# Kernel optimization log

Hardware: AMD Instinct MI355X
Metric: run time of the kernel (lower is better)

The kernel has to match this reference:

```python
import jax, jax.numpy as jnp
import numpy as np

B, S, HID = 2, 4096, 1024
H, D = 16, 64

def rotate_half(x):
    x1, x2 = jnp.split(x, 2, axis=-1)
    return jnp.concatenate([-x2, x1], axis=-1)

def setup_inputs() -> dict:
    key = jax.random.key(0)
    ks = jax.random.split(key, 8)
    hidden_states = jax.random.normal(ks[0], (B, S, HID), dtype=jnp.float32)
    pos = jnp.arange(S, dtype=jnp.float32)[:, None]
    inv_freq = 1.0 / (10000.0 ** (jnp.arange(0, D, 2, dtype=jnp.float32) / D))
    freqs = pos * inv_freq[None, :]
    emb = jnp.concatenate([freqs, freqs], axis=-1)  # [S, D]
    cos = jnp.cos(emb)
    sin = jnp.sin(emb)
    W_rkv = jax.random.normal(ks[1], (3 * H * D, HID), dtype=jnp.float32) * 0.02
    W_o = jax.random.normal(ks[2], (HID, H * D), dtype=jnp.float32) * 0.02
    # match torch init: uniform(-8,-5), uniform(-1,1), uniform(0.2,0.8)
    time_decay = jax.random.uniform(ks[3], (H, D), minval=-8.0, maxval=-5.0, dtype=jnp.float32)
    time_first = jax.random.uniform(ks[4], (H, D), minval=-1.0, maxval=1.0, dtype=jnp.float32)
    time_mix = jax.random.uniform(ks[5], (1, 1, HID), minval=0.2, maxval=0.8, dtype=jnp.float32)
    return {"hidden_states": hidden_states, "cos": cos, "sin": sin,
            "W_rkv": W_rkv, "W_o": W_o, "time_decay": time_decay,
            "time_first": time_first, "time_mix": time_mix}

def reference(hidden_states, cos, sin, W_rkv, W_o, time_decay, time_first, time_mix):
    b, s, hid = hidden_states.shape
    # token-shift time mixing
    xx = jnp.concatenate([jnp.zeros_like(hidden_states[:, :1]), hidden_states[:, :-1]], axis=1)
    mixed = hidden_states * time_mix + xx * (1.0 - time_mix)
    rkv = jnp.einsum('bsh,oh->bso', mixed, W_rkv).reshape(b, s, 3, H, D)
    r = jax.nn.sigmoid(rkv[:, :, 0])  # [B,S,H,D]
    k = rkv[:, :, 1]
    v = rkv[:, :, 2]
    # rotary on r, k
    c = cos[None, :, None, :]
    sn = sin[None, :, None, :]
    r = r * c + rotate_half(r) * sn
    k = k * c + rotate_half(k) * sn
    # fast rwkv linear attention (parallel approximation)
    w = -jnp.exp(time_decay)
    kv = k * v  # [B,S,H,D]
    pos = jnp.arange(s, dtype=hidden_states.dtype)
    pos_diff = pos[:, None] - pos[None, :]  # [S,S]
    mask = pos_diff > 0  # i > j masked (per original code)
    avg_decay = jnp.mean(w)
    pd = jnp.where(mask, 0.0, pos_diff)
    dw = jnp.where(mask, 0.0, jnp.exp(avg_decay * -jnp.abs(pd)))
    dw = dw / (dw.sum(axis=1, keepdims=True) + 1e-8)
    weighted_kv = jnp.einsum('ij,bjhd->bihd', dw, kv)
    out = r * (time_first[None, None] * kv + weighted_kv)  # [B,S,H,D]
    out = out.reshape(b, s, H * D)
    return jnp.einsum('bso,ho->bsh', out, W_o)
```

## Files before the change

### kernel.cpp

```cpp
#include <hip/hip_runtime.h>
#include <math.h>

#define S_LEN 4096
#define HIDN  1024
#define NH    16
#define HD    64
#define BATCH 2
#define M_TOTAL (BATCH * S_LEN)
#define N_RKV   (3 * HIDN)
#define CS 128
#define NC (S_LEN / CS)

typedef __attribute__((ext_vector_type(8))) _Float16 f16x8;
typedef __attribute__((ext_vector_type(4))) float f32x4;
typedef __attribute__((ext_vector_type(4))) unsigned short u16x4;

__device__ __forceinline__ unsigned short f2h(float x) {
    _Float16 h = (_Float16)x;
    return *(unsigned short*)&h;
}
__device__ __forceinline__ float h2f(unsigned short b) {
    _Float16 h = *(_Float16*)&b;
    return (float)h;
}

__device__ __forceinline__ void load_lds16(const void* g, void* l) {
    __builtin_amdgcn_global_load_lds((const __attribute__((address_space(1))) void*)g,
                                     (__attribute__((address_space(3))) void*)l, 16, 0, 0);
}

__global__ __launch_bounds__(256)
void k_split_mix(const float* __restrict__ hs, const float* __restrict__ tm,
                 unsigned short* __restrict__ Ah) {
    int g = blockIdx.x * 256 + threadIdx.x;
    int kc = (g & 255) * 4;
    int m = g >> 8;
    float4 cur = *(const float4*)&hs[(size_t)m * HIDN + kc];
    float4 t4  = *(const float4*)&tm[kc];
    float4 prev = make_float4(0.f, 0.f, 0.f, 0.f);
    if (m & (S_LEN - 1)) prev = *(const float4*)&hs[(size_t)(m - 1) * HIDN + kc];
    u16x4 h;
    h.x = f2h(cur.x * t4.x + prev.x * (1.f - t4.x));
    h.y = f2h(cur.y * t4.y + prev.y * (1.f - t4.y));
    h.z = f2h(cur.z * t4.z + prev.z * (1.f - t4.z));
    h.w = f2h(cur.w * t4.w + prev.w * (1.f - t4.w));
    *(u16x4*)&Ah[(size_t)m * HIDN + kc] = h;
}

__global__ __launch_bounds__(256)
void k_prep_w(const float* __restrict__ Wr, unsigned short* __restrict__ Wrh,
              const float* __restrict__ Wo, unsigned short* __restrict__ Woh,
              const float* __restrict__ td, float* __restrict__ a_out) {
    int bid = blockIdx.x;
    if (bid < 4096) {
        const float* src = (bid < 3072) ? Wr : Wo;
        unsigned short* dst = (bid < 3072) ? Wrh : Woh;
        int g = ((bid < 3072) ? bid : (bid - 3072)) * 256 + threadIdx.x;
        size_t o = (size_t)g * 4;
        float4 v = *(const float4*)&src[o];
        u16x4 h;
        h.x = f2h(v.x); h.y = f2h(v.y); h.z = f2h(v.z); h.w = f2h(v.w);
        *(u16x4*)&dst[o] = h;
    } else if (threadIdx.x < 64) {
        int t = threadIdx.x;
        double acc = 0.0;
        for (int i = t; i < NH * HD; i += 64) acc += exp((double)td[i]);
        for (int off = 32; off > 0; off >>= 1) acc += __shfl_down(acc, off, 64);
        if (t == 0) a_out[0] = (float)(acc / (double)(NH * HD));
    }
}

__device__ __forceinline__ f32x4 mfma16(f16x8 a, f16x8 b, f32x4 c) {
    return __builtin_amdgcn_mfma_f32_16x16x32_f16(a, b, c, 0, 0, 0);
}

#define SBAR  do { __builtin_amdgcn_sched_barrier(0); __builtin_amdgcn_s_barrier(); \
                   __builtin_amdgcn_sched_barrier(0); } while (0)
#define LGKM0 do { asm volatile("s_waitcnt lgkmcnt(0)" ::: "memory"); \
                   __builtin_amdgcn_sched_barrier(0); } while (0)
#define VMC(n) asm volatile("s_waitcnt vmcnt(" #n ")" ::: "memory")

__global__ __launch_bounds__(512, 2)
void k_gemm1_8ph(const unsigned short* __restrict__ A,
                 const unsigned short* __restrict__ Bm,
                 unsigned short* __restrict__ C)
{
    __shared__ unsigned short smem[57344];
    const int tid  = threadIdx.x;
    const int lane = tid & 63;
    const int wv   = tid >> 6;
    const int wm = wv >> 2, wn = wv & 3;
    const int lm = lane & 15, rq = lane >> 4;
    const int swz = (lm & 7) << 4;

    const int cpx = gridDim.x >> 3;
    const int wg  = (blockIdx.x & 7) * cpx + (blockIdx.x >> 3);
    const int bx  = wg & 15;
    const int by  = wg >> 4;
    const int m0 = by * 256, n0 = bx * 192;

    const int srow = 8 * wv + (lane >> 3);
    const int scol = ((lane & 7) ^ (lane >> 3)) * 8;
    const unsigned short* sA = A  + (size_t)(m0 + srow) * 1024 + scol;
    const unsigned short* sB = Bm + (size_t)(n0 + srow) * 1024 + scol;
    unsigned short* dA = smem + wv * 512;
    unsigned short* dB = smem + 16384 + wv * 512;

#define STG_A(u, T, bf) load_lds16(sA + (u)*65536 + (T)*64, dA + (bf)*28672 + (u)*4096)
#define STG_B(u, T, bf) load_lds16(sB + (u)*65536 + (T)*64, dB + (bf)*28672 + (u)*4096)

    const int arow = (wm * 128 + lm) * 128 + rq * 16;
    int boff[3][2];
#pragma unroll
    for (int nt = 0; nt < 3; ++nt)
#pragma unroll
        for (int kk = 0; kk < 2; ++kk)
            boff[nt][kk] = (((wn * 48 + nt * 16 + lm) * 128 + rq * 16 + kk * 64) ^ swz);

    f16x8 aF[2][2], bF[3][2];
    f32x4 acc[8][3] = {};

#define READ_A(q, bf) { const char* Ab = (const char*)smem + (bf)*57344; \
    _Pragma("unroll") for (int m2 = 0; m2 < 2; ++m2) \
    _Pragma("unroll") for (int kk = 0; kk < 2; ++kk) \
        aF[m2][kk] = *(const f16x8*)(Ab + ((arow + (q)*4096 + m2*2048 + kk*64) ^ swz)); }

#define READ_B(bf) { const char* Bb = (const char*)smem + (bf)*57344 + 32768; \
    _Pragma("unroll") for (int nt = 0; nt < 3; ++nt) \
    _Pragma("unroll") for (int kk = 0; kk < 2; ++kk) \
        bF[nt][kk] = *(const f16x8*)(Bb + boff[nt][kk]); }

#define MMQ(q) { __builtin_amdgcn_s_setprio(1); \
    _Pragma("unroll") for (int kk = 0; kk < 2; ++kk) \
    _Pragma("unroll") for (int m2 = 0; m2 < 2; ++m2) \
    _Pragma("unroll") for (int nt = 0; nt < 3; ++nt) \
        acc[(q)*2+m2][nt] = mfma16(aF[m2][kk], bF[nt][kk], acc[(q)*2+m2][nt]); \
    __builtin_amdgcn_s_setprio(0); }

    STG_A(0,0,0); STG_A(1,0,0); STG_A(2,0,0); STG_A(3,0,0);
    STG_B(0,0,0); STG_B(1,0,0); STG_B(2,0,0);
    STG_B(0,1,1); STG_B(1,1,1); STG_B(2,1,1);
    STG_A(0,1,1); STG_A(2,1,1);
    VMC(5);
    SBAR;

    for (int it = 0; it < 8; ++it) {
        const int t = 2 * it;
        const bool st = (it < 7);
        READ_A(0, 0); READ_B(0);
        STG_A(1, t + 1, 1); STG_A(3, t + 1, 1);
        SBAR; LGKM0; MMQ(0); SBAR;
        READ_A(1, 0);
        if (st) { STG_B(0, t + 2, 0); STG_B(1, t + 2, 0); }
        SBAR; LGKM0; MMQ(1); SBAR;
        READ_A(2, 0);
        if (st) { STG_B(2, t + 2, 0); STG_A(0, t + 2, 0); }
        SBAR; LGKM0; MMQ(2); SBAR;
        READ_A(3, 0);
        if (st) { STG_A(2, t + 2, 0); }
        SBAR; LGKM0; MMQ(3);
        if (st) { VMC(5); } else { VMC(0); }
        SBAR;
        READ_A(0, 1); READ_B(1);
        if (st) { STG_A(1, t + 2, 0); STG_A(3, t + 2, 0); }
        SBAR; LGKM0; MMQ(0); SBAR;
        READ_A(1, 1);
        if (st) { STG_B(0, t + 3, 1); STG_B(1, t + 3, 1); }
        SBAR; LGKM0; MMQ(1); SBAR;
        READ_A(2, 1);
        if (st) { STG_B(2, t + 3, 1); STG_A(0, t + 3, 1); }
        SBAR; LGKM0; MMQ(2); SBAR;
        READ_A(3, 1);
        if (st) { STG_A(2, t + 3, 1); }
        SBAR; LGKM0; MMQ(3);
        if (st) { VMC(5); }
        SBAR;
    }

#pragma unroll
    for (int mt = 0; mt < 8; ++mt)
#pragma unroll
        for (int nt = 0; nt < 3; ++nt) {
            int col = n0 + wn * 48 + nt * 16 + lm;
#pragma unroll
            for (int r = 0; r < 4; ++r) {
                int row = m0 + wm * 128 + mt * 16 + rq * 4 + r;
                C[(size_t)row * N_RKV + col] = f2h(acc[mt][nt][r]);
            }
        }
}

template<int LDC, int NBX, bool HALF_OUT>
__global__ __launch_bounds__(256, 2)
void k_gemm_bt(const unsigned short* __restrict__ A,
               const unsigned short* __restrict__ Bm,
               void* __restrict__ Cv)
{
    __shared__ unsigned short smem[16384];
    const int tid  = threadIdx.x;
    const int lane = tid & 63;
    const int wave = tid >> 6;
    const int wm = wave >> 1, wn = wave & 1;

    const int cpx = gridDim.x >> 3;
    const int wg  = (blockIdx.x & 7) * cpx + (blockIdx.x >> 3);
    const int bx  = wg % NBX;
    const int by  = wg / NBX;
    const int m0 = by * 128;
    const int n0 = bx * 128;

    const unsigned short* segsrc[4];
    int segdst[4];
    {
        int rowoff = lane >> 2;
        int q = (lane & 3) ^ (rowoff & 3);
#pragma unroll
        for (int i = 0; i < 4; ++i) {
            int s = wave * 4 + i;
            const unsigned short* base = (s < 8) ? A : Bm;
            int row = (s < 8) ? (m0 + s * 16) : (n0 + (s - 8) * 16);
            segsrc[i] = base + (size_t)(row + rowoff) * 1024 + q * 8;
            segdst[i] = s * 512;
        }
    }

    const int lm = lane & 15;
    const int rq = lane >> 4;
    const int qx = rq ^ (lane & 3);
    int aoff[4], boff2[4];
#pragma unroll
    for (int t = 0; t < 4; ++t) {
        aoff[t]  = (wm * 64 + t * 16 + lm) * 32 + qx * 8;
        boff2[t] = 4096 + (wn * 64 + t * 16 + lm) * 32 + qx * 8;
    }

    f32x4 acc[4][4] = {};

#pragma unroll
    for (int i = 0; i < 4; ++i) load_lds16(segsrc[i], smem + segdst[i]);

    int p = 0;
    for (int kt = 0; kt < 1024; kt += 32) {
        __syncthreads();
        if (kt + 32 < 1024) {
#pragma unroll
            for (int i = 0; i < 4; ++i)
                load_lds16(segsrc[i] + kt + 32, smem + ((p ^ 1) * 8192 + segdst[i]));
        }
        const unsigned short* sb = smem + p * 8192;
        f16x8 fah[4], fb[4];
#pragma unroll
        for (int t = 0; t < 4; ++t) {
            fah[t] = *(const f16x8*)(sb + aoff[t]);
            fb[t]  = *(const f16x8*)(sb + boff2[t]);
        }
#pragma unroll
        for (int mt = 0; mt < 4; ++mt)
#pragma unroll
            for (int nt = 0; nt < 4; ++nt)
                acc[mt][nt] = mfma16(fah[mt], fb[nt], acc[mt][nt]);
        p ^= 1;
    }

#pragma unroll
    for (int mt = 0; mt < 4; ++mt)
#pragma unroll
        for (int nt = 0; nt < 4; ++nt) {
            int col = n0 + wn * 64 + nt * 16 + lm;
#pragma unroll
            for (int r = 0; r < 4; ++r) {
                int row = m0 + wm * 64 + mt * 16 + rq * 4 + r;
                if constexpr (HALF_OUT)
                    ((unsigned short*)Cv)[(size_t)row * LDC + col] = f2h(acc[mt][nt][r]);
                else
                    ((float*)Cv)[(size_t)row * LDC + col] = acc[mt][nt][r];
            }
        }
}

__global__ __launch_bounds__(256)
void k_cb(const unsigned short* __restrict__ rkv,
          const float* __restrict__ cosp, const float* __restrict__ sinp,
          const float* __restrict__ a_ptr, float* __restrict__ Cb)
{
    __shared__ float Ls[4][64][4];
    int bid = blockIdx.x;
    int c  = bid & (NC - 1);
    int bh = bid >> 5;
    int b = bh >> 4, h = bh & 15;
    int lane = threadIdx.x & 63;
    int wave = threadIdx.x >> 6;
    int lm = lane & 15;
    int rs = lane >> 4;
    int d0 = lm * 4;
    float a = a_ptr[0];
    float sgn = (lm < 8) ? -1.f : 1.f;
    float ps0 = 0.f, ps1 = 0.f, ps2 = 0.f, ps3 = 0.f;
#pragma unroll
    for (int it = 0; it < 8; ++it) {
        int t = wave * 32 + it * 4 + rs;
        int s = c * CS + t;
        const unsigned short* rk = rkv + ((size_t)b * S_LEN + s) * N_RKV + h * 64 + d0;
        u16x4 k4 = *(const u16x4*)(rk + 1024);
        u16x4 v4 = *(const u16x4*)(rk + 2048);
        float4 cs4 = *(const float4*)&cosp[s * HD + d0];
        float4 sn4 = *(const float4*)&sinp[s * HD + d0];
        float e = expf(a * (float)t);
        float k0 = h2f(k4.x), k1 = h2f(k4.y), k2 = h2f(k4.z), k3 = h2f(k4.w);
        float kp0 = __shfl_xor(k0, 8, 64);
        float kp1 = __shfl_xor(k1, 8, 64);
        float kp2 = __shfl_xor(k2, 8, 64);
        float kp3 = __shfl_xor(k3, 8, 64);
        ps0 += e * (k0 * cs4.x + sgn * kp0 * sn4.x) * h2f(v4.x);
        ps1 += e * (k1 * cs4.y + sgn * kp1 * sn4.y) * h2f(v4.y);
        ps2 += e * (k2 * cs4.z + sgn * kp2 * sn4.z) * h2f(v4.z);
        ps3 += e * (k3 * cs4.w + sgn * kp3 * sn4.w) * h2f(v4.w);
    }
    Ls[wave][lane][0] = ps0; Ls[wave][lane][1] = ps1;
    Ls[wave][lane][2] = ps2; Ls[wave][lane][3] = ps3;
    __syncthreads();
    if (threadIdx.x < 64) {
        int d = threadIdx.x;
        int lmm = d >> 2, j = d & 3;
        float sum = 0.f;
#pragma unroll
        for (int wvv = 0; wvv < 4; ++wvv)
#pragma unroll
            for (int r = 0; r < 4; ++r)
                sum += Ls[wvv][r * 16 + lmm][j];
        Cb[((size_t)bh * NC + c) * 64 + d] = sum;
    }
}

__global__ __launch_bounds__(64)
void k_chunk_suffix(const float* __restrict__ Cb, const float* __restrict__ a_ptr,
                    float* __restrict__ Sb, float* __restrict__ Zt) {
    int bh = blockIdx.x;
    int d = threadIdx.x;
    float a = a_ptr[0];
    float eaCS = expf(a * (float)CS);
    float run = 0.f;
    Sb[(size_t)(bh * NC + NC - 1) * 64 + d] = 0.f;
    for (int c = NC - 2; c >= 0; --c) {
        run = Cb[(size_t)(bh * NC + c + 1) * 64 + d] + eaCS * run;
        Sb[(size_t)(bh * NC + c) * 64 + d] = run;
    }
    float em1a = expm1f(a);
#pragma unroll
    for (int j = 0; j < 2; ++j) {
        int i = bh * 128 + j * 64 + d;
        Zt[i] = 1.f / (expm1f(a * (float)(S_LEN - i)) / em1a + 1e-8f);
    }
}

__global__ __launch_bounds__(256)
void k_wkv2(const unsigned short* __restrict__ rkv,
            const float* __restrict__ cosp, const float* __restrict__ sinp,
            const float* __restrict__ Sb, const float* __restrict__ a_ptr,
            const float* __restrict__ tf, const float* __restrict__ Zt,
            unsigned short* __restrict__ outH) {
    __shared__ unsigned short L[3 * 128 * 64];
    __shared__ float Tl[4][64];
    int bid = blockIdx.x;
    int c  = bid & (NC - 1);
    int bh = bid >> 5;
    int b = bh >> 4, h = bh & 15;
    int lane = threadIdx.x & 63;
    int wave = threadIdx.x >> 6;
    int s0 = c * CS;

#pragma unroll
    for (int i = 0; i < 12; ++i) {
        int seg = wave * 12 + i;
        int stream = seg >> 4;
        int rg = seg & 15;
        int row = rg * 8 + (lane >> 3);
        const unsigned short* src = rkv
            + ((size_t)b * S_LEN + s0 + row) * N_RKV + stream * 1024 + h * 64
            + (lane & 7) * 8;
        load_lds16(src, L + stream * 8192 + rg * 512);
    }
    __syncthreads();

    float a = a_ptr[0];
    float ea = expf(a);
    const unsigned short* Lr = L;
    const unsigned short* Lk = L + 8192;
    const unsigned short* Lv = L + 16384;
    float sgn = (lane < 32) ? -1.f : 1.f;
    int lx = lane ^ 32;

    float kvreg[32], rreg[32];
    float w = 1.f, T = 0.f;
#pragma unroll
    for (int t = 0; t < 32; ++t) {
        int row = wave * 32 + t;
        float r_ = h2f(Lr[row * 64 + lane]);
        float k_ = h2f(Lk[row * 64 + lane]);
        float kp = h2f(Lk[row * 64 + lx]);
        float v_ = h2f(Lv[row * 64 + lane]);
        float cs = cosp[(s0 + row) * HD + lane];
        float sn = sinp[(s0 + row) * HD + lane];
        float sig = 1.f / (1.f + expf(-r_));
        float sigp = __shfl_xor(sig, 32, 64);
        rreg[t]  = sig * cs + sgn * sigp * sn;
        kvreg[t] = (k_ * cs + sgn * kp * sn) * v_;
        T += w * kvreg[t];
        w *= ea;
    }
    Tl[wave][lane] = T;
    __syncthreads();

    float e32 = expf(a * 32.f);
    float S_run = Sb[(size_t)bid * 64 + lane] * expf(a * 32.f * (float)(3 - wave));
    float f = 1.f;
    for (int wp = wave + 1; wp < 4; ++wp) {
        S_run += f * Tl[wp][lane];
        f *= e32;
    }
    float tfv = tf[h * HD + lane];
#pragma unroll
    for (int t = 31; t >= 0; --t) {
        float kv = kvreg[t];
        S_run = kv + ea * S_run;
        int ig = s0 + wave * 32 + t;
        float o = rreg[t] * (tfv * kv + S_run * Zt[ig]);
        size_t m = (size_t)b * S_LEN + ig;
        outH[m * HIDN + h * HD + lane] = f2h(o);
    }
}

extern "C" void kernel_launch(void* const* d_in, const int* in_sizes, int n_in,
                              void* d_out, int out_size, void* d_ws, size_t ws_size,
                              hipStream_t stream) {
    const float* hs    = (const float*)d_in[0];
    const float* cosp  = (const float*)d_in[1];
    const float* sinp  = (const float*)d_in[2];
    const float* W_rkv = (const float*)d_in[3];
    const float* W_o   = (const float*)d_in[4];
    const float* td    = (const float*)d_in[5];
    const float* tf    = (const float*)d_in[6];
    const float* tm    = (const float*)d_in[7];
    float* out = (float*)d_out;

    char* w = (char*)d_ws;
    unsigned short* rkvH = (unsigned short*)w;
    unsigned short* Ah   = (unsigned short*)(w + 50331648);
    unsigned short* outH = (unsigned short*)(w + 50331648);
    unsigned short* Wrh  = (unsigned short*)(w + 67108864);
    unsigned short* Woh  = (unsigned short*)(w + 73400320);
    float*          Cb   = (float*)(w + 75497472);
    float*          Sb   = (float*)(w + 75759616);
    float*          a_ptr= (float*)(w + 76021760);
    float*          Zt   = (float*)(w + 67108864);

    k_split_mix<<<(M_TOTAL * HIDN / 4) / 256, 256, 0, stream>>>(hs, tm, Ah);
    k_prep_w<<<4097, 256, 0, stream>>>(W_rkv, Wrh, W_o, Woh, td, a_ptr);

    k_gemm1_8ph<<<512, 512, 0, stream>>>(Ah, Wrh, rkvH);

    k_cb<<<BATCH * NH * NC, 256, 0, stream>>>(rkvH, cosp, sinp, a_ptr, Cb);
    k_chunk_suffix<<<BATCH * NH, 64, 0, stream>>>(Cb, a_ptr, Sb, Zt);
    k_wkv2<<<BATCH * NH * NC, 256, 0, stream>>>(rkvH, cosp, sinp, Sb, a_ptr, tf, Zt, outH);

    k_gemm_bt<HIDN, 8, false><<<512, 256, 0, stream>>>(outH, Woh, out);
}
```

Measured before the change: 233.3 us.

## Store rkv in head-planar layout and fold chunk suffix scan into wkv kernel

The first GEMM's epilogue now writes r, k and v into separate planes laid out as [b*h][s][d]. This makes the per-head loads in k_cb and k_wkv2 contiguous 128-byte rows instead of strided slices of a 3072-wide row. The serial k_chunk_suffix kernel is removed. Each wkv block recomputes its own suffix sum over later chunks' Cb, and k_cb computes Zt. The GEMM stores become scattered at 64-element granularity, and wkv does redundant suffix work of up to 31 steps per block.

```diff
diff --git a/kernel.cpp b/kernel.cpp
--- a/kernel.cpp
+++ b/kernel.cpp
@@ -10,6 +10,7 @@
 #define N_RKV   (3 * HIDN)
 #define CS 128
 #define NC (S_LEN / CS)
+#define PLANE 8388608
 
 typedef __attribute__((ext_vector_type(8))) _Float16 f16x8;
 typedef __attribute__((ext_vector_type(4))) float f32x4;
@@ -182,10 +183,17 @@
 #pragma unroll
         for (int nt = 0; nt < 3; ++nt) {
             int col = n0 + wn * 48 + nt * 16 + lm;
+            int stp = col >> 10;
+            int rem = col & 1023;
+            int h   = rem >> 6;
+            int d   = rem & 63;
 #pragma unroll
             for (int r = 0; r < 4; ++r) {
                 int row = m0 + wm * 128 + mt * 16 + rq * 4 + r;
-                C[(size_t)row * N_RKV + col] = f2h(acc[mt][nt][r]);
+                int b = row >> 12, s = row & 4095;
+                size_t addr = (size_t)stp * PLANE
+                            + (((size_t)((b << 4) + h) * 4096 + s) << 6) + d;
+                C[addr] = f2h(acc[mt][nt][r]);
             }
         }
 }
@@ -281,13 +289,13 @@
 __global__ __launch_bounds__(256)
 void k_cb(const unsigned short* __restrict__ rkv,
           const float* __restrict__ cosp, const float* __restrict__ sinp,
-          const float* __restrict__ a_ptr, float* __restrict__ Cb)
+          const float* __restrict__ a_ptr, float* __restrict__ Cb,
+          float* __restrict__ Zt)
 {
     __shared__ float Ls[4][64][4];
     int bid = blockIdx.x;
     int c  = bid & (NC - 1);
     int bh = bid >> 5;
-    int b = bh >> 4, h = bh & 15;
     int lane = threadIdx.x & 63;
     int wave = threadIdx.x >> 6;
     int lm = lane & 15;
@@ -295,14 +303,15 @@
     int d0 = lm * 4;
     float a = a_ptr[0];
     float sgn = (lm < 8) ? -1.f : 1.f;
+    const unsigned short* Kp = rkv + PLANE     + (size_t)bh * 4096 * 64;
+    const unsigned short* Vp = rkv + 2 * PLANE + (size_t)bh * 4096 * 64;
     float ps0 = 0.f, ps1 = 0.f, ps2 = 0.f, ps3 = 0.f;
 #pragma unroll
     for (int it = 0; it < 8; ++it) {
         int t = wave * 32 + it * 4 + rs;
         int s = c * CS + t;
-        const unsigned short* rk = rkv + ((size_t)b * S_LEN + s) * N_RKV + h * 64 + d0;
-        u16x4 k4 = *(const u16x4*)(rk + 1024);
-        u16x4 v4 = *(const u16x4*)(rk + 2048);
+        u16x4 k4 = *(const u16x4*)(Kp + (size_t)s * 64 + d0);
+        u16x4 v4 = *(const u16x4*)(Vp + (size_t)s * 64 + d0);
         float4 cs4 = *(const float4*)&cosp[s * HD + d0];
         float4 sn4 = *(const float4*)&sinp[s * HD + d0];
         float e = expf(a * (float)t);
@@ -330,25 +339,9 @@
                 sum += Ls[wvv][r * 16 + lmm][j];
         Cb[((size_t)bh * NC + c) * 64 + d] = sum;
     }
-}
-
-__global__ __launch_bounds__(64)
-void k_chunk_suffix(const float* __restrict__ Cb, const float* __restrict__ a_ptr,
-                    float* __restrict__ Sb, float* __restrict__ Zt) {
-    int bh = blockIdx.x;
-    int d = threadIdx.x;
-    float a = a_ptr[0];
-    float eaCS = expf(a * (float)CS);
-    float run = 0.f;
-    Sb[(size_t)(bh * NC + NC - 1) * 64 + d] = 0.f;
-    for (int c = NC - 2; c >= 0; --c) {
-        run = Cb[(size_t)(bh * NC + c + 1) * 64 + d] + eaCS * run;
-        Sb[(size_t)(bh * NC + c) * 64 + d] = run;
-    }
-    float em1a = expm1f(a);
-#pragma unroll
-    for (int j = 0; j < 2; ++j) {
-        int i = bh * 128 + j * 64 + d;
+    if (bh == 0 && threadIdx.x >= 128) {
+        int i = c * 128 + (threadIdx.x - 128);
+        float em1a = expm1f(a);
         Zt[i] = 1.f / (expm1f(a * (float)(S_LEN - i)) / em1a + 1e-8f);
     }
 }
@@ -356,7 +349,7 @@
 __global__ __launch_bounds__(256)
 void k_wkv2(const unsigned short* __restrict__ rkv,
             const float* __restrict__ cosp, const float* __restrict__ sinp,
-            const float* __restrict__ Sb, const float* __restrict__ a_ptr,
+            const float* __restrict__ Cb, const float* __restrict__ a_ptr,
             const float* __restrict__ tf, const float* __restrict__ Zt,
             unsigned short* __restrict__ outH) {
     __shared__ unsigned short L[3 * 128 * 64];
@@ -375,9 +368,8 @@
         int stream = seg >> 4;
         int rg = seg & 15;
         int row = rg * 8 + (lane >> 3);
-        const unsigned short* src = rkv
-            + ((size_t)b * S_LEN + s0 + row) * N_RKV + stream * 1024 + h * 64
-            + (lane & 7) * 8;
+        const unsigned short* src = rkv + (size_t)stream * PLANE
+            + ((size_t)bh * 4096 + s0 + row) * 64 + (lane & 7) * 8;
         load_lds16(src, L + stream * 8192 + rg * 512);
     }
     __syncthreads();
@@ -411,8 +403,13 @@
     Tl[wave][lane] = T;
     __syncthreads();
 
+    float eaCS = expf(a * (float)CS);
+    float run = 0.f;
+    for (int cc = NC - 1; cc > c; --cc)
+        run = Cb[((size_t)bh * NC + cc) * 64 + lane] + eaCS * run;
+
     float e32 = expf(a * 32.f);
-    float S_run = Sb[(size_t)bid * 64 + lane] * expf(a * 32.f * (float)(3 - wave));
+    float S_run = run * expf(a * 32.f * (float)(3 - wave));
     float f = 1.f;
     for (int wp = wave + 1; wp < 4; ++wp) {
         S_run += f * Tl[wp][lane];
@@ -450,7 +447,6 @@
     unsigned short* Wrh  = (unsigned short*)(w + 67108864);
     unsigned short* Woh  = (unsigned short*)(w + 73400320);
     float*          Cb   = (float*)(w + 75497472);
-    float*          Sb   = (float*)(w + 75759616);
     float*          a_ptr= (float*)(w + 76021760);
     float*          Zt   = (float*)(w + 67108864);
 
@@ -459,9 +455,8 @@
 
     k_gemm1_8ph<<<512, 512, 0, stream>>>(Ah, Wrh, rkvH);
 
-    k_cb<<<BATCH * NH * NC, 256, 0, stream>>>(rkvH, cosp, sinp, a_ptr, Cb);
-    k_chunk_suffix<<<BATCH * NH, 64, 0, stream>>>(Cb, a_ptr, Sb, Zt);
-    k_wkv2<<<BATCH * NH * NC, 256, 0, stream>>>(rkvH, cosp, sinp, Sb, a_ptr, tf, Zt, outH);
+    k_cb<<<BATCH * NH * NC, 256, 0, stream>>>(rkvH, cosp, sinp, a_ptr, Cb, Zt);
+    k_wkv2<<<BATCH * NH * NC, 256, 0, stream>>>(rkvH, cosp, sinp, Cb, a_ptr, tf, Zt, outH);
 
     k_gemm_bt<HIDN, 8, false><<<512, 256, 0, stream>>>(outH, Woh, out);
 }
```

Result: no change. 236.7 us (+1.5%).
